# Kernel optimization log

Measured on AMD Instinct MI355X. Metric: run time of the kernel, lower is better.

Reference implementation:

```python
import jax, jax.numpy as jnp
import numpy as np

NEG_INF = -1.0e9  # matches masked_fill value in the torch source


def setup_inputs() -> dict:
    key = jax.random.key(0)
    k1, k2, k3, k4 = jax.random.split(key, 4)
    B, H, L, D = 4, 16, 2048, 64
    query = jax.random.normal(k1, (B, H, L, D), dtype=jnp.float32)
    key_t = jax.random.normal(k2, (B, H, L, D), dtype=jnp.float32)
    value = jax.random.normal(k3, (B, H, L, D), dtype=jnp.float32)
    attention_mask = jax.random.randint(k4, (B, L), 0, 2, dtype=jnp.int64)
    return {"query": query, "key": key_t, "value": value, "attention_mask": attention_mask}


def reference(query, key, value, attention_mask):
    d = query.shape[-1]
    scale = 1.0 / jnp.sqrt(jnp.asarray(d, dtype=query.dtype))
    # scores: [B, H, Lq, Lk]
    scores = jnp.einsum("bhqd,bhkd->bhqk", query, key) * scale
    # mask: [B, Lk] -> [B, 1, 1, Lk]; positions where mask == 0 get -1e9
    m = attention_mask[:, None, None, :]
    scores = jnp.where(m == 0, jnp.asarray(NEG_INF, dtype=scores.dtype), scores)
    attn = jax.nn.softmax(scores, axis=-1)
    return jnp.einsum("bhqk,bhkd->bhqd", attn, value)
```

## Files before the change

kernel.cpp:

```cpp
#include <hip/hip_runtime.h>
#include <hip/hip_bf16.h>
#include <stdint.h>

#define B_    4
#define H_    16
#define L_    2048
#define D_    64
#define BH_   64
#define NT_   32
#define MASKBIAS (-1.4426950408889634e9f)

typedef __attribute__((ext_vector_type(8))) short bf16x8;
typedef __attribute__((ext_vector_type(8))) unsigned short ushort8;
typedef __attribute__((ext_vector_type(4))) unsigned short ushort4v;
typedef __attribute__((ext_vector_type(4))) float f32x4;

__device__ __forceinline__ ushort f2bf(float f) {
  union { float f; uint32_t u; } x; x.f = f;
  uint32_t r = x.u + 0x7FFFu + ((x.u >> 16) & 1u);
  return (ushort)(r >> 16);
}

__device__ __forceinline__ uint32_t pkbf(float lo, float hi) {
  uint32_t r;
  asm("v_cvt_pk_bf16_f32 %0, %1, %2" : "=v"(r) : "v"(lo), "v"(hi));
  return r;
}

__global__ __launch_bounds__(256, 2)
void prep_kv(const float* __restrict__ K, const float* __restrict__ V,
             ushort* __restrict__ Kp, ushort* __restrict__ Vtp)
{
  __shared__ ushort Vl[64 * 68];
  const int bid = blockIdx.x;
  const int tid = threadIdx.x;
  const float* Kg = K + (size_t)bid * 4096;
  const float* Vg = V + (size_t)bid * 4096;
  ushort* Kt = Kp + (size_t)bid * 4096;
  ushort* Vt = Vtp + (size_t)bid * 4096;

#pragma unroll
  for (int j = 0; j < 2; ++j) {
    int chunk = j * 256 + tid;
    int row = chunk >> 3, d8 = chunk & 7;
    const float* s = Kg + row * 64 + d8 * 8;
    float4 a = *(const float4*)s, b2 = *(const float4*)(s + 4);
    ushort8 o;
    o[0]=f2bf(a.x); o[1]=f2bf(a.y); o[2]=f2bf(a.z); o[3]=f2bf(a.w);
    o[4]=f2bf(b2.x);o[5]=f2bf(b2.y);o[6]=f2bf(b2.z);o[7]=f2bf(b2.w);
    *(ushort8*)(Kt + row * 64 + ((d8 * 8) ^ ((row & 7) << 3))) = o;

    const float* sv = Vg + row * 64 + d8 * 8;
    float4 va = *(const float4*)sv, vb2 = *(const float4*)(sv + 4);
    ushort4v w0, w1;
    w0[0]=f2bf(va.x); w0[1]=f2bf(va.y); w0[2]=f2bf(va.z); w0[3]=f2bf(va.w);
    w1[0]=f2bf(vb2.x);w1[1]=f2bf(vb2.y);w1[2]=f2bf(vb2.z);w1[3]=f2bf(vb2.w);
    *(ushort4v*)(&Vl[row * 68 + d8 * 8])     = w0;
    *(ushort4v*)(&Vl[row * 68 + d8 * 8 + 4]) = w1;
  }
  __syncthreads();
#pragma unroll
  for (int j = 0; j < 2; ++j) {
    int chunk = j * 256 + tid;
    int d = chunk >> 3, p8 = chunk & 7;
    ushort8 o;
#pragma unroll
    for (int e = 0; e < 8; ++e) {
      int pos = p8 * 8 + e;
      int c = pos >> 5, lgv = (pos >> 3) & 3, bb = (pos >> 2) & 1, aa = pos & 3;
      int kk = 32 * c + 16 * bb + 4 * lgv + aa;
      o[e] = Vl[kk * 68 + d];
    }
    *(ushort8*)(Vt + d * 64 + ((p8 * 8) ^ ((d & 7) << 3))) = o;
  }
}

__global__ __launch_bounds__(256, 4)
void attn_fwd6(const float* __restrict__ Q, const int* __restrict__ Mask,
               const ushort* __restrict__ Kp, const ushort* __restrict__ Vtp,
               float* __restrict__ O)
{
  __shared__ __align__(16) ushort Kb[2][4096];
  __shared__ __align__(16) ushort Vb[2][4096];
  __shared__ __align__(16) float  mb[2][64];

  const int tid  = threadIdx.x;
  const int wid  = tid >> 6;
  const int lane = tid & 63;
  const int lr   = lane & 15;
  const int lg   = lane >> 4;

  const int x   = blockIdx.x;
  const int lin = (x & 7) * 128 + (x >> 3);
  const int bh  = lin >> 4;
  const int qt  = lin & 15;
  const int b   = bh >> 4;

  const float*  Qg    = Q + (size_t)bh * L_ * D_;
  const int*    Mg    = Mask + (size_t)b * L_;
  float*        Og    = O + (size_t)bh * L_ * D_;
  const ushort* Kbase = Kp  + (size_t)bh * 131072;
  const ushort* Vbase = Vtp + (size_t)bh * 131072;

  const int qbase = qt * 128 + wid * 32;
  const float qscale = 0.125f * 1.4426950408889634f;

  bf16x8 qf[2][2];
#pragma unroll
  for (int g = 0; g < 2; ++g)
#pragma unroll
    for (int c = 0; c < 2; ++c) {
      const float* src = Qg + (size_t)(qbase + g * 16 + lr) * D_ + c * 32 + lg * 8;
      float4 a = *(const float4*)src, b2 = *(const float4*)(src + 4);
      bf16x8 q;
      q[0]=f2bf(a.x*qscale);  q[1]=f2bf(a.y*qscale);  q[2]=f2bf(a.z*qscale);  q[3]=f2bf(a.w*qscale);
      q[4]=f2bf(b2.x*qscale); q[5]=f2bf(b2.y*qscale); q[6]=f2bf(b2.z*qscale); q[7]=f2bf(b2.w*qscale);
      qf[g][c] = q;
    }

  f32x4 o_acc[2][4];
#pragma unroll
  for (int g = 0; g < 2; ++g)
#pragma unroll
    for (int dt = 0; dt < 4; ++dt) o_acc[g][dt] = (f32x4){0.f,0.f,0.f,0.f};
  f32x4 l4[2];
#pragma unroll
  for (int g = 0; g < 2; ++g) l4[g] = (f32x4){0.f,0.f,0.f,0.f};

  ushort8 rk0, rk1, rv0, rv1; float rmf = 0.f;
  {
    rk0 = *(const ushort8*)(Kbase + wid * 1024 + lane * 8);
    rk1 = *(const ushort8*)(Kbase + wid * 1024 + 512 + lane * 8);
    rv0 = *(const ushort8*)(Vbase + wid * 1024 + lane * 8);
    rv1 = *(const ushort8*)(Vbase + wid * 1024 + 512 + lane * 8);
    if (tid < 64) rmf = (Mg[tid] != 0) ? 0.f : MASKBIAS;
  }

  int cur = 0;
  for (int kt = 0; kt < NT_; ++kt) {
    *(ushort8*)(&Kb[cur][wid * 1024 + lane * 8])       = rk0;
    *(ushort8*)(&Kb[cur][wid * 1024 + 512 + lane * 8]) = rk1;
    *(ushort8*)(&Vb[cur][wid * 1024 + lane * 8])       = rv0;
    *(ushort8*)(&Vb[cur][wid * 1024 + 512 + lane * 8]) = rv1;
    if (tid < 64) mb[cur][tid] = rmf;

    if (kt + 1 < NT_) {
      const ushort* Ks = Kbase + (size_t)(kt + 1) * 4096;
      const ushort* Vs = Vbase + (size_t)(kt + 1) * 4096;
      rk0 = *(const ushort8*)(Ks + wid * 1024 + lane * 8);
      rk1 = *(const ushort8*)(Ks + wid * 1024 + 512 + lane * 8);
      rv0 = *(const ushort8*)(Vs + wid * 1024 + lane * 8);
      rv1 = *(const ushort8*)(Vs + wid * 1024 + 512 + lane * 8);
      if (tid < 64) rmf = (Mg[(kt + 1) * 64 + tid] != 0) ? 0.f : MASKBIAS;
    }
    __syncthreads();

    const ushort* Kc = Kb[cur];
    const ushort* Vc = Vb[cur];
    const float*  mc = mb[cur];

    f32x4 bt[4];
#pragma unroll
    for (int t = 0; t < 4; ++t) bt[t] = *(const f32x4*)(mc + 16 * t + 4 * lg);

    f32x4 st[2][4];
    {
      bf16x8 kf[4];
#pragma unroll
      for (int t = 0; t < 4; ++t)
        kf[t] = *(const bf16x8*)(Kc + (16 * t + lr) * 64 + ((lg * 8) ^ ((lr & 7) << 3)));
      __builtin_amdgcn_s_setprio(1);
#pragma unroll
      for (int g = 0; g < 2; ++g)
#pragma unroll
        for (int t = 0; t < 4; ++t)
          st[g][t] = __builtin_amdgcn_mfma_f32_16x16x32_bf16(kf[t], qf[g][0], bt[t], 0, 0, 0);
      __builtin_amdgcn_s_setprio(0);
    }
    {
      bf16x8 kf[4];
#pragma unroll
      for (int t = 0; t < 4; ++t)
        kf[t] = *(const bf16x8*)(Kc + (16 * t + lr) * 64 + ((32 + lg * 8) ^ ((lr & 7) << 3)));
      __builtin_amdgcn_s_setprio(1);
#pragma unroll
      for (int g = 0; g < 2; ++g)
#pragma unroll
        for (int t = 0; t < 4; ++t)
          st[g][t] = __builtin_amdgcn_mfma_f32_16x16x32_bf16(kf[t], qf[g][1], st[g][t], 0, 0, 0);
      __builtin_amdgcn_s_setprio(0);
    }

    union PKU { uint32_t u[8]; bf16x8 v[2]; } pk[2];
#pragma unroll
    for (int g = 0; g < 2; ++g) {
      f32x4 p0, p1, p2, p3;
#pragma unroll
      for (int r = 0; r < 4; ++r) {
        p0[r] = __builtin_amdgcn_exp2f(st[g][0][r]);
        p1[r] = __builtin_amdgcn_exp2f(st[g][1][r]);
        p2[r] = __builtin_amdgcn_exp2f(st[g][2][r]);
        p3[r] = __builtin_amdgcn_exp2f(st[g][3][r]);
      }
      l4[g] += (p0 + p1) + (p2 + p3);
      pk[g].u[0] = pkbf(p0[0], p0[1]); pk[g].u[1] = pkbf(p0[2], p0[3]);
      pk[g].u[2] = pkbf(p1[0], p1[1]); pk[g].u[3] = pkbf(p1[2], p1[3]);
      pk[g].u[4] = pkbf(p2[0], p2[1]); pk[g].u[5] = pkbf(p2[2], p2[3]);
      pk[g].u[6] = pkbf(p3[0], p3[1]); pk[g].u[7] = pkbf(p3[2], p3[3]);
    }

    __builtin_amdgcn_s_setprio(1);
#pragma unroll
    for (int c = 0; c < 2; ++c)
#pragma unroll
      for (int dt = 0; dt < 4; ++dt) {
        bf16x8 vb = *(const bf16x8*)(Vc + (16 * dt + lr) * 64 + ((c * 32 + lg * 8) ^ ((lr & 7) << 3)));
#pragma unroll
        for (int g = 0; g < 2; ++g)
          o_acc[g][dt] = __builtin_amdgcn_mfma_f32_16x16x32_bf16(pk[g].v[c], vb, o_acc[g][dt], 0, 0, 0);
      }
    __builtin_amdgcn_s_setprio(0);
    cur ^= 1;
  }

#pragma unroll
  for (int g = 0; g < 2; ++g) {
    float lsum = (l4[g][0] + l4[g][1]) + (l4[g][2] + l4[g][3]);
    lsum += __shfl_xor(lsum, 16);
    lsum += __shfl_xor(lsum, 32);
    float linv[4];
#pragma unroll
    for (int r = 0; r < 4; ++r) {
      float lq = __shfl(lsum, 20 * lg + r);
      linv[r] = 1.0f / lq;
    }
#pragma unroll
    for (int dt = 0; dt < 4; ++dt)
#pragma unroll
      for (int r = 0; r < 4; ++r) {
        int row = qbase + g * 16 + 4 * lg + r;
        Og[(size_t)row * D_ + dt * 16 + lr] = o_acc[g][dt][r] * linv[r];
      }
  }
}

extern "C" void kernel_launch(void* const* d_in, const int* in_sizes, int n_in,
                              void* d_out, int out_size, void* d_ws, size_t ws_size,
                              hipStream_t stream) {
  const float* Q = (const float*)d_in[0];
  const float* K = (const float*)d_in[1];
  const float* V = (const float*)d_in[2];
  const int*   M = (const int*)d_in[3];
  float*       O = (float*)d_out;

  const size_t elems = (size_t)BH_ * L_ * D_;
  ushort* Kp  = (ushort*)d_ws;
  ushort* Vtp = Kp + elems;
  prep_kv<<<dim3(BH_ * NT_), dim3(256), 0, stream>>>(K, V, Kp, Vtp);
  attn_fwd6<<<dim3(1024), dim3(256), 0, stream>>>(Q, M, Kp, Vtp, O);
}
```

Measured before the change: 109.1 us.

## Stream K/V tiles directly into LDS and precompute mask bias in prep

Replaces the register-staged K/V double buffering with global_load_lds direct-to-LDS copies. Each iteration now ends with a vmcnt wait plus a barrier instead of a store-then-syncthreads step. The mask-to-bias conversion moves into the prep kernel and is read straight from global memory each tile. V fragments are loaded into registers before the softmax so the PV MFMAs no longer wait on LDS reads. This cuts VGPR pressure and LDS store instructions, but the wait sits at the end of each iteration and puts the global load latency in the critical path. It also adds per-tile global reads for the mask bias.

```diff
diff --git a/kernel.cpp b/kernel.cpp
--- a/kernel.cpp
+++ b/kernel.cpp
@@ -27,9 +27,17 @@
   return r;
 }
 
+__device__ __forceinline__ void gload16(const ushort* g, ushort* l) {
+  __builtin_amdgcn_global_load_lds(
+      (const __attribute__((address_space(1))) uint32_t*)g,
+      (__attribute__((address_space(3))) uint32_t*)l, 16, 0, 0);
+}
+
 __global__ __launch_bounds__(256, 2)
 void prep_kv(const float* __restrict__ K, const float* __restrict__ V,
-             ushort* __restrict__ Kp, ushort* __restrict__ Vtp)
+             const int* __restrict__ Mask,
+             ushort* __restrict__ Kp, ushort* __restrict__ Vtp,
+             float* __restrict__ Mb)
 {
   __shared__ ushort Vl[64 * 68];
   const int bid = blockIdx.x;
@@ -73,16 +81,20 @@
     }
     *(ushort8*)(Vt + d * 64 + ((p8 * 8) ^ ((d & 7) << 3))) = o;
   }
+  if ((((bid >> 5) & 15) == 0) && tid < 64) {
+    int b = bid >> 9, kt = bid & 31;
+    int idx = b * 2048 + kt * 64 + tid;
+    Mb[idx] = (Mask[idx] != 0) ? 0.f : MASKBIAS;
+  }
 }
 
 __global__ __launch_bounds__(256, 4)
-void attn_fwd6(const float* __restrict__ Q, const int* __restrict__ Mask,
+void attn_fwd7(const float* __restrict__ Q, const float* __restrict__ Mb,
                const ushort* __restrict__ Kp, const ushort* __restrict__ Vtp,
                float* __restrict__ O)
 {
   __shared__ __align__(16) ushort Kb[2][4096];
   __shared__ __align__(16) ushort Vb[2][4096];
-  __shared__ __align__(16) float  mb[2][64];
 
   const int tid  = threadIdx.x;
   const int wid  = tid >> 6;
@@ -97,10 +109,10 @@
   const int b   = bh >> 4;
 
   const float*  Qg    = Q + (size_t)bh * L_ * D_;
-  const int*    Mg    = Mask + (size_t)b * L_;
   float*        Og    = O + (size_t)bh * L_ * D_;
   const ushort* Kbase = Kp  + (size_t)bh * 131072;
   const ushort* Vbase = Vtp + (size_t)bh * 131072;
+  const float*  Mbb   = Mb + (size_t)b * L_;
 
   const int qbase = qt * 128 + wid * 32;
   const float qscale = 0.125f * 1.4426950408889634f;
@@ -127,41 +139,32 @@
 #pragma unroll
   for (int g = 0; g < 2; ++g) l4[g] = (f32x4){0.f,0.f,0.f,0.f};
 
-  ushort8 rk0, rk1, rv0, rv1; float rmf = 0.f;
-  {
-    rk0 = *(const ushort8*)(Kbase + wid * 1024 + lane * 8);
-    rk1 = *(const ushort8*)(Kbase + wid * 1024 + 512 + lane * 8);
-    rv0 = *(const ushort8*)(Vbase + wid * 1024 + lane * 8);
-    rv1 = *(const ushort8*)(Vbase + wid * 1024 + 512 + lane * 8);
-    if (tid < 64) rmf = (Mg[tid] != 0) ? 0.f : MASKBIAS;
-  }
+  gload16(Kbase +        wid * 512 + lane * 8, &Kb[0][       wid * 512]);
+  gload16(Kbase + 2048 + wid * 512 + lane * 8, &Kb[0][2048 + wid * 512]);
+  gload16(Vbase +        wid * 512 + lane * 8, &Vb[0][       wid * 512]);
+  gload16(Vbase + 2048 + wid * 512 + lane * 8, &Vb[0][2048 + wid * 512]);
+  asm volatile("s_waitcnt vmcnt(0)" ::: "memory");
+  __builtin_amdgcn_s_barrier();
+  __builtin_amdgcn_sched_barrier(0);
 
   int cur = 0;
   for (int kt = 0; kt < NT_; ++kt) {
-    *(ushort8*)(&Kb[cur][wid * 1024 + lane * 8])       = rk0;
-    *(ushort8*)(&Kb[cur][wid * 1024 + 512 + lane * 8]) = rk1;
-    *(ushort8*)(&Vb[cur][wid * 1024 + lane * 8])       = rv0;
-    *(ushort8*)(&Vb[cur][wid * 1024 + 512 + lane * 8]) = rv1;
-    if (tid < 64) mb[cur][tid] = rmf;
+    f32x4 bt[4];
+#pragma unroll
+    for (int t = 0; t < 4; ++t)
+      bt[t] = *(const f32x4*)(Mbb + kt * 64 + 16 * t + 4 * lg);
 
     if (kt + 1 < NT_) {
       const ushort* Ks = Kbase + (size_t)(kt + 1) * 4096;
       const ushort* Vs = Vbase + (size_t)(kt + 1) * 4096;
-      rk0 = *(const ushort8*)(Ks + wid * 1024 + lane * 8);
-      rk1 = *(const ushort8*)(Ks + wid * 1024 + 512 + lane * 8);
-      rv0 = *(const ushort8*)(Vs + wid * 1024 + lane * 8);
-      rv1 = *(const ushort8*)(Vs + wid * 1024 + 512 + lane * 8);
-      if (tid < 64) rmf = (Mg[(kt + 1) * 64 + tid] != 0) ? 0.f : MASKBIAS;
-    }
-    __syncthreads();
+      gload16(Ks +        wid * 512 + lane * 8, &Kb[cur ^ 1][       wid * 512]);
+      gload16(Ks + 2048 + wid * 512 + lane * 8, &Kb[cur ^ 1][2048 + wid * 512]);
+      gload16(Vs +        wid * 512 + lane * 8, &Vb[cur ^ 1][       wid * 512]);
+      gload16(Vs + 2048 + wid * 512 + lane * 8, &Vb[cur ^ 1][2048 + wid * 512]);
+    }
 
     const ushort* Kc = Kb[cur];
     const ushort* Vc = Vb[cur];
-    const float*  mc = mb[cur];
-
-    f32x4 bt[4];
-#pragma unroll
-    for (int t = 0; t < 4; ++t) bt[t] = *(const f32x4*)(mc + 16 * t + 4 * lg);
 
     f32x4 st[2][4];
     {
@@ -190,6 +193,13 @@
           st[g][t] = __builtin_amdgcn_mfma_f32_16x16x32_bf16(kf[t], qf[g][1], st[g][t], 0, 0, 0);
       __builtin_amdgcn_s_setprio(0);
     }
+
+    bf16x8 vb[4][2];
+#pragma unroll
+    for (int dt = 0; dt < 4; ++dt)
+#pragma unroll
+      for (int c = 0; c < 2; ++c)
+        vb[dt][c] = *(const bf16x8*)(Vc + (16 * dt + lr) * 64 + ((c * 32 + lg * 8) ^ ((lr & 7) << 3)));
 
     union PKU { uint32_t u[8]; bf16x8 v[2]; } pk[2];
 #pragma unroll
@@ -213,13 +223,15 @@
 #pragma unroll
     for (int c = 0; c < 2; ++c)
 #pragma unroll
-      for (int dt = 0; dt < 4; ++dt) {
-        bf16x8 vb = *(const bf16x8*)(Vc + (16 * dt + lr) * 64 + ((c * 32 + lg * 8) ^ ((lr & 7) << 3)));
+      for (int dt = 0; dt < 4; ++dt)
 #pragma unroll
         for (int g = 0; g < 2; ++g)
-          o_acc[g][dt] = __builtin_amdgcn_mfma_f32_16x16x32_bf16(pk[g].v[c], vb, o_acc[g][dt], 0, 0, 0);
-      }
+          o_acc[g][dt] = __builtin_amdgcn_mfma_f32_16x16x32_bf16(pk[g].v[c], vb[dt][c], o_acc[g][dt], 0, 0, 0);
     __builtin_amdgcn_s_setprio(0);
+
+    asm volatile("s_waitcnt vmcnt(0)" ::: "memory");
+    __builtin_amdgcn_s_barrier();
+    __builtin_amdgcn_sched_barrier(0);
     cur ^= 1;
   }
 
@@ -256,6 +268,7 @@
   const size_t elems = (size_t)BH_ * L_ * D_;
   ushort* Kp  = (ushort*)d_ws;
   ushort* Vtp = Kp + elems;
-  prep_kv<<<dim3(BH_ * NT_), dim3(256), 0, stream>>>(K, V, Kp, Vtp);
-  attn_fwd6<<<dim3(1024), dim3(256), 0, stream>>>(Q, M, Kp, Vtp, O);
-}
+  float*  Mb  = (float*)(Vtp + elems);
+  prep_kv<<<dim3(BH_ * NT_), dim3(256), 0, stream>>>(K, V, M, Kp, Vtp, Mb);
+  attn_fwd7<<<dim3(1024), dim3(256), 0, stream>>>(Q, Mb, Kp, Vtp, O);
+}
```

After: 117.0 us. 7.3% more time.
